# Optimization experiments

Hardware: AMD Instinct MI355X
Metric: run time of the kernel (lower is better)

The kernel has to match this reference:

```python
import jax, jax.numpy as jnp
import numpy as np

N = 50000   # num_nodes
E = 800000  # num_edges
IN, HID, OUT = 64, 96, 96
LN_EPS = 1e-5


def setup_inputs() -> dict:
    key = jax.random.key(0)
    ks = jax.random.split(key, 12)
    s = 0.05
    return {
        "x": jax.random.normal(ks[0], (N, IN), jnp.float32),
        "edge_index": jax.random.randint(ks[1], (2, E), 0, N, dtype=jnp.int64),
        "edge_weight": jax.random.uniform(ks[2], (E,), jnp.float32),
        "W0": jax.random.normal(ks[3], (IN, HID), jnp.float32) * s,
        "b0": jnp.zeros((HID,), jnp.float32),
        "ln_g": jnp.ones((HID,), jnp.float32),
        "ln_b": jnp.zeros((HID,), jnp.float32),
        "Ws": jax.random.normal(ks[4], (IN, HID), jnp.float32) * s,
        "bs": jnp.zeros((HID,), jnp.float32),
        "W1": jax.random.normal(ks[5], (HID, OUT), jnp.float32) * s,
        "b1": jnp.zeros((OUT,), jnp.float32),
    }


def _gcn(h, W, b, src, dst, ew, n):
    # GCNConv with add_self_loops=True and edge weights (PyG gcn_norm)
    loop = jnp.arange(n, dtype=src.dtype)
    s = jnp.concatenate([src, loop])
    d = jnp.concatenate([dst, loop])
    w = jnp.concatenate([ew, jnp.ones((n,), ew.dtype)])
    deg = jax.ops.segment_sum(w, d, num_segments=n)
    dinv = jnp.where(deg > 0, jax.lax.rsqrt(jnp.maximum(deg, 1e-12)), 0.0)
    norm = dinv[s] * w * dinv[d]                 # [E+N]
    msg = (h @ W)[s] * norm[:, None]             # gather transformed src feats
    return jax.ops.segment_sum(msg, d, num_segments=n) + b


def _layernorm(h, g, b):
    mu = h.mean(-1, keepdims=True)
    var = ((h - mu) ** 2).mean(-1, keepdims=True)
    return (h - mu) * jax.lax.rsqrt(var + LN_EPS) * g + b


def reference(x, edge_index, edge_weight, W0, b0, ln_g, ln_b, Ws, bs, W1, b1):
    src, dst = edge_index[0], edge_index[1]
    n = x.shape[0]
    # layer 0: GCN -> LayerNorm -> ReLU -> (dropout: eval no-op) -> +Linear skip
    h = _gcn(x, W0, b0, src, dst, edge_weight, n)
    h = jax.nn.relu(_layernorm(h, ln_g, ln_b))
    h = h + (x @ Ws + bs)
    # final layer: GCN only
    return _gcn(h, W1, b1, src, dst, edge_weight, n)
```

## Files before the change

### kernel.cpp

```cpp
#include <hip/hip_runtime.h>

#define LN_EPS 1e-5f

__device__ __forceinline__ float bflo(unsigned u) { union { unsigned u; float f; } c; c.u = u << 16; return c.f; }
__device__ __forceinline__ float bfhi(unsigned u) { union { unsigned u; float f; } c; c.u = u & 0xffff0000u; return c.f; }
__device__ __forceinline__ unsigned f2bfbits(float f) {
    union { float f; unsigned u; } c; c.f = f;
    return (c.u + 0x7fffu + ((c.u >> 16) & 1u)) >> 16;
}
__device__ __forceinline__ unsigned packbf(float lo, float hi) {
    return f2bfbits(lo) | (f2bfbits(hi) << 16);
}

__global__ void init_kernel(int* __restrict__ cnt, int n) {
    int i = blockIdx.x * 256 + threadIdx.x;
    if (i < n) cnt[i] = 0;
}

__global__ void cnt_part_kernel(const int* __restrict__ dst, int* __restrict__ cnt,
                                int e, int n) {
    int part = blockIdx.x & 7;
    int blk  = blockIdx.x >> 3;
    int chunk = (n + 7) >> 3;
    int lo = part * chunk;
    int hi = lo + chunk; if (hi > n) hi = n;
    int stride = (gridDim.x >> 3) * 256;
    for (int i = blk * 256 + threadIdx.x; i < e; i += stride) {
        int d = dst[i];
        if (d >= lo && d < hi) atomicAdd(&cnt[d], 1);
    }
}

__global__ void cvt_x_kernel(const float* __restrict__ x, unsigned* __restrict__ xb2, int total4) {
    int i = blockIdx.x * 256 + threadIdx.x;
    if (i >= total4) return;
    float4 v = ((const float4*)x)[i];
    uint2 o;
    o.x = packbf(v.x, v.y);
    o.y = packbf(v.z, v.w);
    ((uint2*)xb2)[i] = o;
}

__global__ void prep_w_kernel(const float* __restrict__ W0, const float* __restrict__ Ws,
                              const float* __restrict__ W1,
                              float4* __restrict__ w0i, float4* __restrict__ wsi,
                              float4* __restrict__ w1i) {
    int i = blockIdx.x * 256 + threadIdx.x;
    if (i < 1536) {
        int kq = i / 96, j = i % 96;
        const float* p = W0 + kq * 4 * 96 + j;
        w0i[i] = make_float4(p[0], p[96], p[192], p[288]);
        const float* q = Ws + kq * 4 * 96 + j;
        wsi[i] = make_float4(q[0], q[96], q[192], q[288]);
    }
    int i2 = i - 1536;
    if (i2 >= 0 && i2 < 2304) {
        int kq = i2 / 96, j = i2 % 96;
        const float* p = W1 + kq * 4 * 96 + j;
        w1i[i2] = make_float4(p[0], p[96], p[192], p[288]);
    }
}

__global__ void blocksum_kernel(const int* __restrict__ cnt, int* __restrict__ bsum, int n) {
    int base = blockIdx.x * 1024;
    int t = threadIdx.x;
    int i0 = base + t * 4;
    int s = 0;
    if (i0 + 3 < n) { int4 v = *(const int4*)(cnt + i0); s = v.x + v.y + v.z + v.w; }
    else { for (int k = 0; k < 4; ++k) if (i0 + k < n) s += cnt[i0 + k]; }
    #pragma unroll
    for (int off = 32; off; off >>= 1) s += __shfl_xor(s, off);
    __shared__ int wsum[4];
    if ((t & 63) == 0) wsum[t >> 6] = s;
    __syncthreads();
    if (t == 0) bsum[blockIdx.x] = wsum[0] + wsum[1] + wsum[2] + wsum[3];
}

__global__ void scan_bsum_kernel(const int* __restrict__ bsum, int* __restrict__ boff, int nb) {
    int t = threadIdx.x;
    int carry = 0;
    for (int base = 0; base < nb; base += 64) {
        int i = base + t;
        int v = (i < nb) ? bsum[i] : 0;
        int sc = v;
        #pragma unroll
        for (int off = 1; off < 64; off <<= 1) {
            int u = __shfl_up(sc, off);
            if (t >= off) sc += u;
        }
        if (i < nb) boff[i] = carry + sc - v;
        carry += __shfl(sc, 63);
    }
}

__global__ void rowptr_kernel(const int* __restrict__ cnt, const int* __restrict__ boff,
                              int* __restrict__ rowptr, int* __restrict__ rowcur,
                              int n, int etot) {
    __shared__ int wsum[4];
    int b = blockIdx.x;
    int t = threadIdx.x;
    int i0 = b * 1024 + t * 4;
    int c0 = 0, c1 = 0, c2 = 0, c3 = 0;
    if (i0 < n)     c0 = cnt[i0];
    if (i0 + 1 < n) c1 = cnt[i0 + 1];
    if (i0 + 2 < n) c2 = cnt[i0 + 2];
    if (i0 + 3 < n) c3 = cnt[i0 + 3];
    int tot = c0 + c1 + c2 + c3;
    int lane = t & 63, w = t >> 6;
    int sc = tot;
    #pragma unroll
    for (int off = 1; off < 64; off <<= 1) {
        int u = __shfl_up(sc, off);
        if (lane >= off) sc += u;
    }
    if (lane == 63) wsum[w] = sc;
    __syncthreads();
    int woff = 0;
    for (int k = 0; k < w; ++k) woff += wsum[k];
    int excl = boff[b] + woff + sc - tot;
    if (i0 < n)     { rowptr[i0]     = excl;             rowcur[i0]     = excl; }
    if (i0 + 1 < n) { rowptr[i0 + 1] = excl + c0;        rowcur[i0 + 1] = excl + c0; }
    if (i0 + 2 < n) { rowptr[i0 + 2] = excl + c0 + c1;   rowcur[i0 + 2] = excl + c0 + c1; }
    if (i0 + 3 < n) { rowptr[i0 + 3] = excl + c0 + c1 + c2; rowcur[i0 + 3] = excl + c0 + c1 + c2; }
    if (b == 0 && t == 0) rowptr[n] = etot;
}

__global__ void scatter_part_kernel(const int* __restrict__ src, const int* __restrict__ dst,
                                    const float* __restrict__ ew,
                                    int* __restrict__ rowcur,
                                    uint2* __restrict__ cv, int e, int n) {
    int part = blockIdx.x & 7;
    int blk  = blockIdx.x >> 3;
    int chunk = (n + 7) >> 3;
    int lo = part * chunk;
    int hi = lo + chunk; if (hi > n) hi = n;
    int stride = (gridDim.x >> 3) * 256;
    for (int i = blk * 256 + threadIdx.x; i < e; i += stride) {
        int d = dst[i];
        if (d >= lo && d < hi) {
            int s = src[i];
            float w = ew[i];
            int pos = atomicAdd(&rowcur[d], 1);
            cv[pos] = make_uint2((unsigned)s, __float_as_uint(w));
        }
    }
}

__global__ void degsum_kernel(const int* __restrict__ rowptr, const uint2* __restrict__ cv,
                              float* __restrict__ dinv, int n) {
    int i = blockIdx.x * 256 + threadIdx.x;
    if (i >= n) return;
    int p0 = rowptr[i], p1 = rowptr[i + 1];
    float s = 1.0f;
    for (int p = p0; p < p1; ++p) s += __uint_as_float(cv[p].y);
    dinv[i] = rsqrtf(s);
}

__global__ void rescale_kernel(const float* __restrict__ dinv, uint2* __restrict__ cv, int e) {
    int i = blockIdx.x * 256 + threadIdx.x;
    if (i >= e) return;
    uint2 v = cv[i];
    v.y = __float_as_uint(__uint_as_float(v.y) * dinv[v.x]);
    cv[i] = v;
}

__global__ void agg64_kernel(const unsigned* __restrict__ xb, const float* __restrict__ dinv,
                             const int* __restrict__ rowptr, const uint2* __restrict__ cv,
                             float* __restrict__ aggX, int n) {
    int node = blockIdx.x * 4 + (threadIdx.x >> 6);
    if (node >= n) return;
    int lane = threadIdx.x & 63;
    int g = lane >> 4, l4 = lane & 15;
    const uint2* x2 = (const uint2*)xb;
    int p0 = rowptr[node], pe = rowptr[node + 1];
    float a0 = 0, a1 = 0, a2 = 0, a3 = 0;
    float b0 = 0, b1 = 0, b2 = 0, b3 = 0;
    for (int p = p0 + g; p < pe; p += 8) {
        uint2 e1 = cv[p];
        int s1 = (int)e1.x; float w1 = __uint_as_float(e1.y);
        uint2 r1 = x2[(size_t)s1 * 16 + l4];
        bool h2 = (p + 4) < pe;
        uint2 e2 = h2 ? cv[p + 4] : e1;
        int s2 = (int)e2.x;
        float w2 = h2 ? __uint_as_float(e2.y) : 0.0f;
        uint2 r2 = x2[(size_t)s2 * 16 + l4];
        a0 = fmaf(w1, bflo(r1.x), a0); a1 = fmaf(w1, bfhi(r1.x), a1);
        a2 = fmaf(w1, bflo(r1.y), a2); a3 = fmaf(w1, bfhi(r1.y), a3);
        b0 = fmaf(w2, bflo(r2.x), b0); b1 = fmaf(w2, bfhi(r2.x), b1);
        b2 = fmaf(w2, bflo(r2.y), b2); b3 = fmaf(w2, bfhi(r2.y), b3);
    }
    a0 += b0; a1 += b1; a2 += b2; a3 += b3;
    #pragma unroll
    for (int off = 16; off <= 32; off <<= 1) {
        a0 += __shfl_xor(a0, off);
        a1 += __shfl_xor(a1, off);
        a2 += __shfl_xor(a2, off);
        a3 += __shfl_xor(a3, off);
    }
    if (g == 0) {
        float di = dinv[node];
        uint2 sr = x2[(size_t)node * 16 + l4];
        a0 = fmaf(di, bflo(sr.x), a0); a1 = fmaf(di, bfhi(sr.x), a1);
        a2 = fmaf(di, bflo(sr.y), a2); a3 = fmaf(di, bfhi(sr.y), a3);
        ((float4*)(aggX + (size_t)node * 64))[l4] =
            make_float4(a0 * di, a1 * di, a2 * di, a3 * di);
    }
}

__global__ __launch_bounds__(512) void gemm_ln_kernel(
        const float4* __restrict__ w0i, const float4* __restrict__ wsi,
        const float* __restrict__ aggX, const float* __restrict__ x,
        const float* __restrict__ b0,
        const float* __restrict__ ln_g, const float* __restrict__ ln_b,
        const float* __restrict__ bs,
        unsigned short* __restrict__ hb, int n) {
    __shared__ float4 w0s[1536];
    __shared__ float4 wss[1536];
    __shared__ float4 ar[1024];
    __shared__ float4 xr[1024];
    int t = threadIdx.x;
    int base = blockIdx.x * 64;
    for (int i = t; i < 1536; i += 512) { w0s[i] = w0i[i]; wss[i] = wsi[i]; }
    int rem = n - base; if (rem > 64) rem = 64;
    int nf4 = rem * 16;
    for (int i = t; i < nf4; i += 512) {
        ar[i] = ((const float4*)(aggX + (size_t)base * 64))[i];
        xr[i] = ((const float4*)(x + (size_t)base * 64))[i];
    }
    __syncthreads();
    int hw = t >> 5;
    int l = t & 31;
    int r0 = hw * 4;
    float acc[4][3] = {{0.f,0.f,0.f},{0.f,0.f,0.f},{0.f,0.f,0.f},{0.f,0.f,0.f}};
    float sk[4][3]  = {{0.f,0.f,0.f},{0.f,0.f,0.f},{0.f,0.f,0.f},{0.f,0.f,0.f}};
    for (int kq = 0; kq < 16; ++kq) {
        float4 wa = w0s[kq * 96 + l];
        float4 wb = w0s[kq * 96 + l + 32];
        float4 wc = w0s[kq * 96 + l + 64];
        float4 sa = wss[kq * 96 + l];
        float4 sb = wss[kq * 96 + l + 32];
        float4 scv = wss[kq * 96 + l + 64];
        #pragma unroll
        for (int r = 0; r < 4; ++r) {
            float4 a  = ar[(r0 + r) * 16 + kq];
            float4 xv = xr[(r0 + r) * 16 + kq];
            acc[r][0] = fmaf(a.w, wa.w, fmaf(a.z, wa.z, fmaf(a.y, wa.y, fmaf(a.x, wa.x, acc[r][0]))));
            acc[r][1] = fmaf(a.w, wb.w, fmaf(a.z, wb.z, fmaf(a.y, wb.y, fmaf(a.x, wb.x, acc[r][1]))));
            acc[r][2] = fmaf(a.w, wc.w, fmaf(a.z, wc.z, fmaf(a.y, wc.y, fmaf(a.x, wc.x, acc[r][2]))));
            sk[r][0]  = fmaf(xv.w, sa.w, fmaf(xv.z, sa.z, fmaf(xv.y, sa.y, fmaf(xv.x, sa.x, sk[r][0]))));
            sk[r][1]  = fmaf(xv.w, sb.w, fmaf(xv.z, sb.z, fmaf(xv.y, sb.y, fmaf(xv.x, sb.x, sk[r][1]))));
            sk[r][2]  = fmaf(xv.w, scv.w, fmaf(xv.z, scv.z, fmaf(xv.y, scv.y, fmaf(xv.x, scv.x, sk[r][2]))));
        }
    }
    float b00 = b0[l], b01 = b0[l + 32], b02 = b0[l + 64];
    float g0 = ln_g[l], g1 = ln_g[l + 32], g2 = ln_g[l + 64];
    float e0 = ln_b[l], e1 = ln_b[l + 32], e2 = ln_b[l + 64];
    float q0 = bs[l],   q1 = bs[l + 32],   q2 = bs[l + 64];
    #pragma unroll
    for (int r = 0; r < 4; ++r) {
        int node = base + r0 + r;
        if (node >= n) break;
        float a0v = acc[r][0] + b00, a1v = acc[r][1] + b01, a2v = acc[r][2] + b02;
        float s1 = a0v + a1v + a2v;
        #pragma unroll
        for (int off = 1; off < 32; off <<= 1) s1 += __shfl_xor(s1, off);
        float mu = s1 * (1.0f / 96.0f);
        float d0 = a0v - mu, d1 = a1v - mu, d2 = a2v - mu;
        float sq = d0 * d0 + d1 * d1 + d2 * d2;
        #pragma unroll
        for (int off = 1; off < 32; off <<= 1) sq += __shfl_xor(sq, off);
        float rinv = rsqrtf(sq * (1.0f / 96.0f) + LN_EPS);
        float v0 = fmaxf(d0 * rinv * g0 + e0, 0.0f) + sk[r][0] + q0;
        float v1 = fmaxf(d1 * rinv * g1 + e1, 0.0f) + sk[r][1] + q1;
        float v2 = fmaxf(d2 * rinv * g2 + e2, 0.0f) + sk[r][2] + q2;
        unsigned short* o = hb + (size_t)node * 128;
        o[l]      = (unsigned short)f2bfbits(v0);
        o[l + 32] = (unsigned short)f2bfbits(v1);
        o[l + 64] = (unsigned short)f2bfbits(v2);
        o[l + 96] = 0;
    }
}

__global__ void agg96_kernel(const unsigned short* __restrict__ hb, const float* __restrict__ dinv,
                             const int* __restrict__ rowptr, const uint2* __restrict__ cv,
                             float* __restrict__ aggH, int n) {
    int node = blockIdx.x * 4 + (threadIdx.x >> 6);
    if (node >= n) return;
    int lane = threadIdx.x & 63;
    int g = lane >> 4, l4 = lane & 15;
    const uint4* h4 = (const uint4*)hb;
    int p0 = rowptr[node], pe = rowptr[node + 1];
    float a0=0,a1=0,a2=0,a3=0,a4=0,a5=0,a6=0,a7=0;
    float c0=0,c1=0,c2=0,c3=0,c4=0,c5=0,c6=0,c7=0;
    for (int p = p0 + g; p < pe; p += 8) {
        uint2 e1 = cv[p];
        int s1 = (int)e1.x; float w1 = __uint_as_float(e1.y);
        uint4 r1 = h4[(size_t)s1 * 16 + l4];
        bool h2 = (p + 4) < pe;
        uint2 e2 = h2 ? cv[p + 4] : e1;
        int s2 = (int)e2.x;
        float w2 = h2 ? __uint_as_float(e2.y) : 0.0f;
        uint4 r2 = h4[(size_t)s2 * 16 + l4];
        a0 = fmaf(w1, bflo(r1.x), a0); a1 = fmaf(w1, bfhi(r1.x), a1);
        a2 = fmaf(w1, bflo(r1.y), a2); a3 = fmaf(w1, bfhi(r1.y), a3);
        a4 = fmaf(w1, bflo(r1.z), a4); a5 = fmaf(w1, bfhi(r1.z), a5);
        a6 = fmaf(w1, bflo(r1.w), a6); a7 = fmaf(w1, bfhi(r1.w), a7);
        c0 = fmaf(w2, bflo(r2.x), c0); c1 = fmaf(w2, bfhi(r2.x), c1);
        c2 = fmaf(w2, bflo(r2.y), c2); c3 = fmaf(w2, bfhi(r2.y), c3);
        c4 = fmaf(w2, bflo(r2.z), c4); c5 = fmaf(w2, bfhi(r2.z), c5);
        c6 = fmaf(w2, bflo(r2.w), c6); c7 = fmaf(w2, bfhi(r2.w), c7);
    }
    a0+=c0; a1+=c1; a2+=c2; a3+=c3; a4+=c4; a5+=c5; a6+=c6; a7+=c7;
    #pragma unroll
    for (int off = 16; off <= 32; off <<= 1) {
        a0 += __shfl_xor(a0, off); a1 += __shfl_xor(a1, off);
        a2 += __shfl_xor(a2, off); a3 += __shfl_xor(a3, off);
        a4 += __shfl_xor(a4, off); a5 += __shfl_xor(a5, off);
        a6 += __shfl_xor(a6, off); a7 += __shfl_xor(a7, off);
    }
    if (g == 0 && l4 < 12) {
        float di = dinv[node];
        uint4 sr = h4[(size_t)node * 16 + l4];
        a0 = fmaf(di, bflo(sr.x), a0); a1 = fmaf(di, bfhi(sr.x), a1);
        a2 = fmaf(di, bflo(sr.y), a2); a3 = fmaf(di, bfhi(sr.y), a3);
        a4 = fmaf(di, bflo(sr.z), a4); a5 = fmaf(di, bfhi(sr.z), a5);
        a6 = fmaf(di, bflo(sr.w), a6); a7 = fmaf(di, bfhi(sr.w), a7);
        float4* o = (float4*)(aggH + (size_t)node * 96);
        o[l4 * 2]     = make_float4(a0 * di, a1 * di, a2 * di, a3 * di);
        o[l4 * 2 + 1] = make_float4(a4 * di, a5 * di, a6 * di, a7 * di);
    }
}

__global__ __launch_bounds__(512) void gemm_out_kernel(
        const float4* __restrict__ w1i, const float* __restrict__ aggH,
        const float* __restrict__ b1, float* __restrict__ out, int n) {
    __shared__ float4 w1s[2304];
    __shared__ float4 hr[1536];
    int t = threadIdx.x;
    int base = blockIdx.x * 64;
    for (int i = t; i < 2304; i += 512) w1s[i] = w1i[i];
    int rem = n - base; if (rem > 64) rem = 64;
    int nf4 = rem * 24;
    for (int i = t; i < nf4; i += 512)
        hr[i] = ((const float4*)(aggH + (size_t)base * 96))[i];
    __syncthreads();
    int hw = t >> 5, l = t & 31;
    int r0 = hw * 4;
    float acc[4][3] = {{0.f,0.f,0.f},{0.f,0.f,0.f},{0.f,0.f,0.f},{0.f,0.f,0.f}};
    for (int kq = 0; kq < 24; ++kq) {
        float4 wa = w1s[kq * 96 + l];
        float4 wb = w1s[kq * 96 + l + 32];
        float4 wc = w1s[kq * 96 + l + 64];
        #pragma unroll
        for (int r = 0; r < 4; ++r) {
            float4 a = hr[(r0 + r) * 24 + kq];
            acc[r][0] = fmaf(a.w, wa.w, fmaf(a.z, wa.z, fmaf(a.y, wa.y, fmaf(a.x, wa.x, acc[r][0]))));
            acc[r][1] = fmaf(a.w, wb.w, fmaf(a.z, wb.z, fmaf(a.y, wb.y, fmaf(a.x, wb.x, acc[r][1]))));
            acc[r][2] = fmaf(a.w, wc.w, fmaf(a.z, wc.z, fmaf(a.y, wc.y, fmaf(a.x, wc.x, acc[r][2]))));
        }
    }
    float c0 = b1[l], c1 = b1[l + 32], c2 = b1[l + 64];
    #pragma unroll
    for (int r = 0; r < 4; ++r) {
        int node = base + r0 + r;
        if (node >= n) break;
        float* o = out + (size_t)node * 96;
        o[l]      = acc[r][0] + c0;
        o[l + 32] = acc[r][1] + c1;
        o[l + 64] = acc[r][2] + c2;
    }
}

extern "C" void kernel_launch(void* const* d_in, const int* in_sizes, int n_in,
                              void* d_out, int out_size, void* d_ws, size_t ws_size,
                              hipStream_t stream) {
    const float* x    = (const float*)d_in[0];
    const int*   ei   = (const int*)d_in[1];
    const float* ew   = (const float*)d_in[2];
    const float* W0   = (const float*)d_in[3];
    const float* b0   = (const float*)d_in[4];
    const float* ln_g = (const float*)d_in[5];
    const float* ln_b = (const float*)d_in[6];
    const float* Ws   = (const float*)d_in[7];
    const float* bs   = (const float*)d_in[8];
    const float* W1   = (const float*)d_in[9];
    const float* b1   = (const float*)d_in[10];
    float* out = (float*)d_out;

    const int E = in_sizes[2];
    const int N = in_sizes[0] / 64;
    const int* src = ei;
    const int* dst = ei + E;

    char* ws = (char*)d_ws;
    size_t off = 0;
    auto alloc = [&](size_t bytes) -> void* {
        void* p = ws + off;
        off = (off + bytes + 255) & ~(size_t)255;
        return p;
    };
    float* dinv   = (float*)alloc((size_t)N * 4);
    int*   cnt    = (int*)alloc((size_t)N * 4);
    int*   rowptr = (int*)alloc((size_t)(N + 1) * 4);
    int*   rowcur = (int*)alloc((size_t)N * 4);
    int*   bsum   = (int*)alloc((size_t)256 * 4);
    int*   boff   = (int*)alloc((size_t)256 * 4);
    uint2* cv     = (uint2*)alloc((size_t)E * 8);
    unsigned* xb  = (unsigned*)alloc((size_t)N * 64 * 2);
    unsigned short* hb = (unsigned short*)alloc((size_t)N * 128 * 2);
    float* bufA   = (float*)alloc((size_t)N * 96 * 4);
    float4* w0i   = (float4*)alloc((size_t)1536 * 16);
    float4* wsi   = (float4*)alloc((size_t)1536 * 16);
    float4* w1i   = (float4*)alloc((size_t)2304 * 16);

    int gN = (N + 255) / 256;
    int gE = (E + 255) / 256;
    int nb = (N + 1023) / 1024;
    int gP = 8 * 128;

    init_kernel<<<gN, 256, 0, stream>>>(cnt, N);
    cnt_part_kernel<<<gP, 256, 0, stream>>>(dst, cnt, E, N);
    cvt_x_kernel<<<(N * 16 + 255) / 256, 256, 0, stream>>>(x, xb, N * 16);
    prep_w_kernel<<<15, 256, 0, stream>>>(W0, Ws, W1, w0i, wsi, w1i);
    blocksum_kernel<<<nb, 256, 0, stream>>>(cnt, bsum, N);
    scan_bsum_kernel<<<1, 64, 0, stream>>>(bsum, boff, nb);
    rowptr_kernel<<<nb, 256, 0, stream>>>(cnt, boff, rowptr, rowcur, N, E);
    scatter_part_kernel<<<gP, 256, 0, stream>>>(src, dst, ew, rowcur, cv, E, N);
    degsum_kernel<<<gN, 256, 0, stream>>>(rowptr, cv, dinv, N);
    rescale_kernel<<<gE, 256, 0, stream>>>(dinv, cv, E);

    int gA = (N + 3) / 4;
    agg64_kernel<<<gA, 256, 0, stream>>>(xb, dinv, rowptr, cv, bufA, N);

    int gG = (N + 63) / 64;
    gemm_ln_kernel<<<gG, 512, 0, stream>>>(w0i, wsi, bufA, x, b0, ln_g, ln_b, bs, hb, N);

    agg96_kernel<<<gA, 256, 0, stream>>>(hb, dinv, rowptr, cv, bufA, N);

    gemm_out_kernel<<<gG, 512, 0, stream>>>(w1i, bufA, b1, out, N);
}
```

Measured before the change: 239.1 us.

## Record per-edge rank during counting, drop rescale pass, and shrink hidden stride

```diff
diff --git a/kernel.cpp b/kernel.cpp
--- a/kernel.cpp
+++ b/kernel.cpp
@@ -17,47 +17,41 @@
     if (i < n) cnt[i] = 0;
 }
 
-__global__ void cnt_part_kernel(const int* __restrict__ dst, int* __restrict__ cnt,
-                                int e, int n) {
-    int part = blockIdx.x & 7;
-    int blk  = blockIdx.x >> 3;
-    int chunk = (n + 7) >> 3;
-    int lo = part * chunk;
-    int hi = lo + chunk; if (hi > n) hi = n;
-    int stride = (gridDim.x >> 3) * 256;
-    for (int i = blk * 256 + threadIdx.x; i < e; i += stride) {
-        int d = dst[i];
-        if (d >= lo && d < hi) atomicAdd(&cnt[d], 1);
-    }
-}
-
-__global__ void cvt_x_kernel(const float* __restrict__ x, unsigned* __restrict__ xb2, int total4) {
+__global__ void cnt_rank_kernel(const int* __restrict__ dst, int* __restrict__ cnt,
+                                int* __restrict__ rank, int e) {
     int i = blockIdx.x * 256 + threadIdx.x;
-    if (i >= total4) return;
-    float4 v = ((const float4*)x)[i];
-    uint2 o;
-    o.x = packbf(v.x, v.y);
-    o.y = packbf(v.z, v.w);
-    ((uint2*)xb2)[i] = o;
-}
-
-__global__ void prep_w_kernel(const float* __restrict__ W0, const float* __restrict__ Ws,
-                              const float* __restrict__ W1,
-                              float4* __restrict__ w0i, float4* __restrict__ wsi,
-                              float4* __restrict__ w1i) {
-    int i = blockIdx.x * 256 + threadIdx.x;
-    if (i < 1536) {
-        int kq = i / 96, j = i % 96;
-        const float* p = W0 + kq * 4 * 96 + j;
-        w0i[i] = make_float4(p[0], p[96], p[192], p[288]);
-        const float* q = Ws + kq * 4 * 96 + j;
-        wsi[i] = make_float4(q[0], q[96], q[192], q[288]);
-    }
-    int i2 = i - 1536;
-    if (i2 >= 0 && i2 < 2304) {
-        int kq = i2 / 96, j = i2 % 96;
-        const float* p = W1 + kq * 4 * 96 + j;
-        w1i[i2] = make_float4(p[0], p[96], p[192], p[288]);
+    if (i >= e) return;
+    rank[i] = atomicAdd(&cnt[dst[i]], 1);
+}
+
+__global__ void cvtprep_kernel(const float* __restrict__ x, unsigned* __restrict__ xb2, int total4,
+                               const float* __restrict__ W0, const float* __restrict__ Ws,
+                               const float* __restrict__ W1,
+                               float4* __restrict__ w0i, float4* __restrict__ wsi,
+                               float4* __restrict__ w1i, int gX) {
+    if ((int)blockIdx.x < gX) {
+        int i = blockIdx.x * 256 + threadIdx.x;
+        if (i >= total4) return;
+        float4 v = ((const float4*)x)[i];
+        uint2 o;
+        o.x = packbf(v.x, v.y);
+        o.y = packbf(v.z, v.w);
+        ((uint2*)xb2)[i] = o;
+    } else {
+        int i = (blockIdx.x - gX) * 256 + threadIdx.x;
+        if (i < 1536) {
+            int kq = i / 96, j = i % 96;
+            const float* p = W0 + kq * 4 * 96 + j;
+            w0i[i] = make_float4(p[0], p[96], p[192], p[288]);
+            const float* q = Ws + kq * 4 * 96 + j;
+            wsi[i] = make_float4(q[0], q[96], q[192], q[288]);
+        }
+        int i2 = i - 1536;
+        if (i2 >= 0 && i2 < 2304) {
+            int kq = i2 / 96, j = i2 % 96;
+            const float* p = W1 + kq * 4 * 96 + j;
+            w1i[i2] = make_float4(p[0], p[96], p[192], p[288]);
+        }
     }
 }
 
@@ -94,8 +88,7 @@
 }
 
 __global__ void rowptr_kernel(const int* __restrict__ cnt, const int* __restrict__ boff,
-                              int* __restrict__ rowptr, int* __restrict__ rowcur,
-                              int n, int etot) {
+                              int* __restrict__ rowptr, int n, int etot) {
     __shared__ int wsum[4];
     int b = blockIdx.x;
     int t = threadIdx.x;
@@ -118,16 +111,16 @@
     int woff = 0;
     for (int k = 0; k < w; ++k) woff += wsum[k];
     int excl = boff[b] + woff + sc - tot;
-    if (i0 < n)     { rowptr[i0]     = excl;             rowcur[i0]     = excl; }
-    if (i0 + 1 < n) { rowptr[i0 + 1] = excl + c0;        rowcur[i0 + 1] = excl + c0; }
-    if (i0 + 2 < n) { rowptr[i0 + 2] = excl + c0 + c1;   rowcur[i0 + 2] = excl + c0 + c1; }
-    if (i0 + 3 < n) { rowptr[i0 + 3] = excl + c0 + c1 + c2; rowcur[i0 + 3] = excl + c0 + c1 + c2; }
+    if (i0 < n)     rowptr[i0]     = excl;
+    if (i0 + 1 < n) rowptr[i0 + 1] = excl + c0;
+    if (i0 + 2 < n) rowptr[i0 + 2] = excl + c0 + c1;
+    if (i0 + 3 < n) rowptr[i0 + 3] = excl + c0 + c1 + c2;
     if (b == 0 && t == 0) rowptr[n] = etot;
 }
 
 __global__ void scatter_part_kernel(const int* __restrict__ src, const int* __restrict__ dst,
-                                    const float* __restrict__ ew,
-                                    int* __restrict__ rowcur,
+                                    const float* __restrict__ ew, const int* __restrict__ rank,
+                                    const int* __restrict__ rowptr,
                                     uint2* __restrict__ cv, int e, int n) {
     int part = blockIdx.x & 7;
     int blk  = blockIdx.x >> 3;
@@ -138,10 +131,8 @@
     for (int i = blk * 256 + threadIdx.x; i < e; i += stride) {
         int d = dst[i];
         if (d >= lo && d < hi) {
-            int s = src[i];
-            float w = ew[i];
-            int pos = atomicAdd(&rowcur[d], 1);
-            cv[pos] = make_uint2((unsigned)s, __float_as_uint(w));
+            int pos = rowptr[d] + rank[i];
+            cv[pos] = make_uint2((unsigned)src[i], __float_as_uint(ew[i]));
         }
     }
 }
@@ -154,14 +145,6 @@
     float s = 1.0f;
     for (int p = p0; p < p1; ++p) s += __uint_as_float(cv[p].y);
     dinv[i] = rsqrtf(s);
-}
-
-__global__ void rescale_kernel(const float* __restrict__ dinv, uint2* __restrict__ cv, int e) {
-    int i = blockIdx.x * 256 + threadIdx.x;
-    if (i >= e) return;
-    uint2 v = cv[i];
-    v.y = __float_as_uint(__uint_as_float(v.y) * dinv[v.x]);
-    cv[i] = v;
 }
 
 __global__ void agg64_kernel(const unsigned* __restrict__ xb, const float* __restrict__ dinv,
@@ -177,12 +160,13 @@
     float b0 = 0, b1 = 0, b2 = 0, b3 = 0;
     for (int p = p0 + g; p < pe; p += 8) {
         uint2 e1 = cv[p];
-        int s1 = (int)e1.x; float w1 = __uint_as_float(e1.y);
+        int s1 = (int)e1.x;
+        float w1 = __uint_as_float(e1.y) * dinv[s1];
         uint2 r1 = x2[(size_t)s1 * 16 + l4];
         bool h2 = (p + 4) < pe;
         uint2 e2 = h2 ? cv[p + 4] : e1;
         int s2 = (int)e2.x;
-        float w2 = h2 ? __uint_as_float(e2.y) : 0.0f;
+        float w2 = h2 ? __uint_as_float(e2.y) * dinv[s2] : 0.0f;
         uint2 r2 = x2[(size_t)s2 * 16 + l4];
         a0 = fmaf(w1, bflo(r1.x), a0); a1 = fmaf(w1, bfhi(r1.x), a1);
         a2 = fmaf(w1, bflo(r1.y), a2); a3 = fmaf(w1, bfhi(r1.y), a3);
@@ -273,11 +257,10 @@
         float v0 = fmaxf(d0 * rinv * g0 + e0, 0.0f) + sk[r][0] + q0;
         float v1 = fmaxf(d1 * rinv * g1 + e1, 0.0f) + sk[r][1] + q1;
         float v2 = fmaxf(d2 * rinv * g2 + e2, 0.0f) + sk[r][2] + q2;
-        unsigned short* o = hb + (size_t)node * 128;
+        unsigned short* o = hb + (size_t)node * 96;
         o[l]      = (unsigned short)f2bfbits(v0);
         o[l + 32] = (unsigned short)f2bfbits(v1);
         o[l + 64] = (unsigned short)f2bfbits(v2);
-        o[l + 96] = 0;
     }
 }
 
@@ -291,26 +274,29 @@
     const uint4* h4 = (const uint4*)hb;
     int p0 = rowptr[node], pe = rowptr[node + 1];
     float a0=0,a1=0,a2=0,a3=0,a4=0,a5=0,a6=0,a7=0;
-    float c0=0,c1=0,c2=0,c3=0,c4=0,c5=0,c6=0,c7=0;
-    for (int p = p0 + g; p < pe; p += 8) {
-        uint2 e1 = cv[p];
-        int s1 = (int)e1.x; float w1 = __uint_as_float(e1.y);
-        uint4 r1 = h4[(size_t)s1 * 16 + l4];
-        bool h2 = (p + 4) < pe;
-        uint2 e2 = h2 ? cv[p + 4] : e1;
-        int s2 = (int)e2.x;
-        float w2 = h2 ? __uint_as_float(e2.y) : 0.0f;
-        uint4 r2 = h4[(size_t)s2 * 16 + l4];
-        a0 = fmaf(w1, bflo(r1.x), a0); a1 = fmaf(w1, bfhi(r1.x), a1);
-        a2 = fmaf(w1, bflo(r1.y), a2); a3 = fmaf(w1, bfhi(r1.y), a3);
-        a4 = fmaf(w1, bflo(r1.z), a4); a5 = fmaf(w1, bfhi(r1.z), a5);
-        a6 = fmaf(w1, bflo(r1.w), a6); a7 = fmaf(w1, bfhi(r1.w), a7);
-        c0 = fmaf(w2, bflo(r2.x), c0); c1 = fmaf(w2, bfhi(r2.x), c1);
-        c2 = fmaf(w2, bflo(r2.y), c2); c3 = fmaf(w2, bfhi(r2.y), c3);
-        c4 = fmaf(w2, bflo(r2.z), c4); c5 = fmaf(w2, bfhi(r2.z), c5);
-        c6 = fmaf(w2, bflo(r2.w), c6); c7 = fmaf(w2, bfhi(r2.w), c7);
-    }
-    a0+=c0; a1+=c1; a2+=c2; a3+=c3; a4+=c4; a5+=c5; a6+=c6; a7+=c7;
+    if (l4 < 12) {
+        float c0=0,c1=0,c2=0,c3=0,c4=0,c5=0,c6=0,c7=0;
+        for (int p = p0 + g; p < pe; p += 8) {
+            uint2 e1 = cv[p];
+            int s1 = (int)e1.x;
+            float w1 = __uint_as_float(e1.y) * dinv[s1];
+            uint4 r1 = h4[(size_t)s1 * 12 + l4];
+            bool h2 = (p + 4) < pe;
+            uint2 e2 = h2 ? cv[p + 4] : e1;
+            int s2 = (int)e2.x;
+            float w2 = h2 ? __uint_as_float(e2.y) * dinv[s2] : 0.0f;
+            uint4 r2 = h4[(size_t)s2 * 12 + l4];
+            a0 = fmaf(w1, bflo(r1.x), a0); a1 = fmaf(w1, bfhi(r1.x), a1);
+            a2 = fmaf(w1, bflo(r1.y), a2); a3 = fmaf(w1, bfhi(r1.y), a3);
+            a4 = fmaf(w1, bflo(r1.z), a4); a5 = fmaf(w1, bfhi(r1.z), a5);
+            a6 = fmaf(w1, bflo(r1.w), a6); a7 = fmaf(w1, bfhi(r1.w), a7);
+            c0 = fmaf(w2, bflo(r2.x), c0); c1 = fmaf(w2, bfhi(r2.x), c1);
+            c2 = fmaf(w2, bflo(r2.y), c2); c3 = fmaf(w2, bfhi(r2.y), c3);
+            c4 = fmaf(w2, bflo(r2.z), c4); c5 = fmaf(w2, bfhi(r2.z), c5);
+            c6 = fmaf(w2, bflo(r2.w), c6); c7 = fmaf(w2, bfhi(r2.w), c7);
+        }
+        a0+=c0; a1+=c1; a2+=c2; a3+=c3; a4+=c4; a5+=c5; a6+=c6; a7+=c7;
+    }
     #pragma unroll
     for (int off = 16; off <= 32; off <<= 1) {
         a0 += __shfl_xor(a0, off); a1 += __shfl_xor(a1, off);
@@ -320,7 +306,7 @@
     }
     if (g == 0 && l4 < 12) {
         float di = dinv[node];
-        uint4 sr = h4[(size_t)node * 16 + l4];
+        uint4 sr = h4[(size_t)node * 12 + l4];
         a0 = fmaf(di, bflo(sr.x), a0); a1 = fmaf(di, bfhi(sr.x), a1);
         a2 = fmaf(di, bflo(sr.y), a2); a3 = fmaf(di, bfhi(sr.y), a3);
         a4 = fmaf(di, bflo(sr.z), a4); a5 = fmaf(di, bfhi(sr.z), a5);
@@ -402,12 +388,12 @@
     float* dinv   = (float*)alloc((size_t)N * 4);
     int*   cnt    = (int*)alloc((size_t)N * 4);
     int*   rowptr = (int*)alloc((size_t)(N + 1) * 4);
-    int*   rowcur = (int*)alloc((size_t)N * 4);
+    int*   rank   = (int*)alloc((size_t)E * 4);
     int*   bsum   = (int*)alloc((size_t)256 * 4);
     int*   boff   = (int*)alloc((size_t)256 * 4);
     uint2* cv     = (uint2*)alloc((size_t)E * 8);
     unsigned* xb  = (unsigned*)alloc((size_t)N * 64 * 2);
-    unsigned short* hb = (unsigned short*)alloc((size_t)N * 128 * 2);
+    unsigned short* hb = (unsigned short*)alloc((size_t)N * 96 * 2);
     float* bufA   = (float*)alloc((size_t)N * 96 * 4);
     float4* w0i   = (float4*)alloc((size_t)1536 * 16);
     float4* wsi   = (float4*)alloc((size_t)1536 * 16);
@@ -416,18 +402,17 @@
     int gN = (N + 255) / 256;
     int gE = (E + 255) / 256;
     int nb = (N + 1023) / 1024;
+    int gX = (N * 16 + 255) / 256;
     int gP = 8 * 128;
 
     init_kernel<<<gN, 256, 0, stream>>>(cnt, N);
-    cnt_part_kernel<<<gP, 256, 0, stream>>>(dst, cnt, E, N);
-    cvt_x_kernel<<<(N * 16 + 255) / 256, 256, 0, stream>>>(x, xb, N * 16);
-    prep_w_kernel<<<15, 256, 0, stream>>>(W0, Ws, W1, w0i, wsi, w1i);
+    cnt_rank_kernel<<<gE, 256, 0, stream>>>(dst, cnt, rank, E);
+    cvtprep_kernel<<<gX + 15, 256, 0, stream>>>(x, xb, N * 16, W0, Ws, W1, w0i, wsi, w1i, gX);
     blocksum_kernel<<<nb, 256, 0, stream>>>(cnt, bsum, N);
     scan_bsum_kernel<<<1, 64, 0, stream>>>(bsum, boff, nb);
-    rowptr_kernel<<<nb, 256, 0, stream>>>(cnt, boff, rowptr, rowcur, N, E);
-    scatter_part_kernel<<<gP, 256, 0, stream>>>(src, dst, ew, rowcur, cv, E, N);
+    rowptr_kernel<<<nb, 256, 0, stream>>>(cnt, boff, rowptr, N, E);
+    scatter_part_kernel<<<gP, 256, 0, stream>>>(src, dst, ew, rank, rowptr, cv, E, N);
     degsum_kernel<<<gN, 256, 0, stream>>>(rowptr, cv, dinv, N);
-    rescale_kernel<<<gE, 256, 0, stream>>>(dinv, cv, E);
 
     int gA = (N + 3) / 4;
     agg64_kernel<<<gA, 256, 0, stream>>>(xb, dinv, rowptr, cv, bufA, N);
```

Result: faster. 218.4 us (-8.7%).
